# Kernel tuning notes

Hardware: AMD Instinct MI355X
Metric: run time of the kernel (lower is better)

## Reference

```python
import jax, jax.numpy as jnp
import numpy as np

BQ = 64  # query block size
BK = 64  # key block size
PV_SCALE = 1e-3  # pvthreshd (~0..50) -> prob threshold, mirrors int8 P-quantization cutoff


def setup_inputs() -> dict:
    key = jax.random.key(0)
    ks = jax.random.split(key, 6)
    B, H, L, D = 2, 16, 2048, 64
    q = jax.random.normal(ks[0], (B, H, L, D), jnp.float32)
    k = jax.random.normal(ks[1], (B, H, L, D), jnp.float32)
    v = jax.random.normal(ks[2], (B, H, L, D), jnp.float32)
    # per-head tuned thresholds (init defaults / autotune ranges)
    cdfthreshd = 0.85 + 0.14 * jax.random.uniform(ks[3], (H,), jnp.float32)
    simthreshd1 = jax.random.uniform(ks[4], (H,), jnp.float32, minval=-0.3, maxval=0.5)
    pvthreshd = jax.random.uniform(ks[5], (H,), jnp.float32, minval=15.0, maxval=25.0)
    return dict(q=q, k=k, v=v, cdfthreshd=cdfthreshd,
                simthreshd1=simthreshd1, pvthreshd=pvthreshd)


def _sparse_meansim_attention(q, k, v, cdfthreshd, simthreshd1, pvthreshd):
    B, H, L, D = q.shape
    nqb, nkb = L // BQ, L // BK
    scale = 1.0 / jnp.sqrt(jnp.float32(D))

    # smooth_k: subtract per-(B,H) key mean along sequence
    k = k - k.mean(axis=2, keepdims=True)

    qb = q.reshape(B, H, nqb, BQ, D)
    kb = k.reshape(B, H, nkb, BK, D)
    qm = qb.mean(axis=3)  # [B,H,nqb,D]
    km = kb.mean(axis=3)  # [B,H,nkb,D]

    # mean cosine similarity of queries to their block mean -> pooled (prunable) blocks
    qn = jnp.linalg.norm(qb, axis=-1)            # [B,H,nqb,BQ]
    qmn = jnp.linalg.norm(qm, axis=-1)           # [B,H,nqb]
    cos = jnp.einsum('bhnqd,bhnd->bhnq', qb, qm) / (qn * qmn[..., None] + 1e-6)
    pooled = cos.mean(axis=-1) > simthreshd1[None, :, None]  # [B,H,nqb]

    # block-level score map from pooled means, CDF-based top-mass block selection
    s = jnp.einsum('bhid,bhjd->bhij', qm, km) * scale        # [B,H,nqb,nkb]
    p = jax.nn.softmax(s, axis=-1)
    order = jnp.argsort(-p, axis=-1)
    p_sorted = jnp.take_along_axis(p, order, axis=-1)
    excl_cdf = jnp.cumsum(p_sorted, axis=-1) - p_sorted      # exclusive CDF
    keep_sorted = excl_cdf < cdfthreshd[None, :, None, None]
    keep = jnp.take_along_axis(keep_sorted, jnp.argsort(order, axis=-1), axis=-1)

    sink = (jnp.arange(nkb) == 0)  # attention_sink: always keep first key block
    block_mask = keep | (~pooled)[..., None] | sink          # [B,H,nqb,nkb]

    # full attention restricted to selected blocks
    S = jnp.einsum('bhqd,bhkd->bhqk', q, k) * scale          # [B,H,L,L]
    m = jnp.repeat(jnp.repeat(block_mask, BQ, axis=2), BK, axis=3)
    P = jax.nn.softmax(jnp.where(m, S, -jnp.inf), axis=-1)

    # second-stage PV pruning: skip PV accumulation for negligible prob blocks
    Pb = P.reshape(B, H, nqb, BQ, nkb, BK)
    pv_keep = Pb.max(axis=(3, 5)) >= pvthreshd[None, :, None, None] * PV_SCALE
    pv_keep = pv_keep | sink
    Pb = Pb * pv_keep[:, :, :, None, :, None].astype(P.dtype)

    o = jnp.einsum('bhqk,bhkd->bhqd', Pb.reshape(B, H, L, L), v)
    return o


def reference(q, k, v, cdfthreshd, simthreshd1, pvthreshd):
    return _sparse_meansim_attention(q, k, v, cdfthreshd, simthreshd1, pvthreshd)
```

## Files before the change

### kernel.cpp

```cpp
#include <hip/hip_runtime.h>
#include <hip/hip_bf16.h>
#include <math.h>
#include <stdint.h>

#define B 2
#define H 16
#define L 2048
#define D 64
#define NB 32

typedef unsigned short u16;
typedef unsigned int u32;
typedef __attribute__((ext_vector_type(2))) unsigned int u32x2;
typedef __attribute__((ext_vector_type(4))) unsigned int u32x4;
typedef __attribute__((ext_vector_type(8))) short s16x8;
typedef __attribute__((ext_vector_type(4))) float f32x4;

union FragU { s16x8 v; u32 u[4]; };

#if defined(__has_builtin)
#if __has_builtin(__builtin_amdgcn_exp2f)
#define EXP2F __builtin_amdgcn_exp2f
#else
#define EXP2F exp2f
#endif
#else
#define EXP2F exp2f
#endif
#define LOG2E 1.4426950408889634f
#define C1SC 0.18033688011112042f

__device__ __forceinline__ u32 pkbf(float a, float b) {
  __hip_bfloat162 h = __float22bfloat162_rn(make_float2(a, b));
  union { __hip_bfloat162 h; u32 u; } cv; cv.h = h; return cv.u;
}
__device__ __forceinline__ float bf2f(u32 u16bits) {
  union { u32 u; float f; } c; c.u = u16bits << 16; return c.f;
}
__device__ __forceinline__ void split4(float4 p, u32x2& hi, u32x2& lo) {
  u32 h01 = pkbf(p.x, p.y), h23 = pkbf(p.z, p.w);
  float rx = p.x - bf2f(h01 & 0xffffu);
  float ry = p.y - bf2f(h01 >> 16);
  float rz = p.z - bf2f(h23 & 0xffffu);
  float rw = p.w - bf2f(h23 >> 16);
  hi = (u32x2){h01, h23};
  lo = (u32x2){pkbf(rx, ry), pkbf(rz, rw)};
}
__device__ __forceinline__ int swz(int row, int colb) {
  return (row << 7) + (colb ^ ((row & 7) << 4));
}

__global__ __launch_bounds__(256) void k_prep(const float* __restrict__ k,
                                              const float* __restrict__ v,
                                              float* __restrict__ ksum,
                                              u16* __restrict__ khi_g,
                                              u16* __restrict__ klo_g,
                                              u16* __restrict__ vthi_g,
                                              u16* __restrict__ vtlo_g,
                                              float* __restrict__ kbmax) {
  int blk0 = blockIdx.x, t = threadIdx.x;
  int xcd = blk0 & 7, sidx = blk0 >> 3;
  int bh = xcd * 4 + (sidx >> 5), j = sidx & 31;
  int blk = bh * 32 + j;
  int lane = t & 63, w = t >> 6;
  __shared__ float vt[64 * 65];
  __shared__ float pk_[4][64];
  __shared__ unsigned bmaxS;
  if (t == 0) bmaxS = 0u;
  size_t base = (size_t)blk * 4096;

  int r0 = t >> 3;
  int c8 = (t & 7) * 8;
  float cs[8] = {0.f, 0.f, 0.f, 0.f, 0.f, 0.f, 0.f, 0.f};
  float rmax = 0.f;
#pragma unroll
  for (int it = 0; it < 2; ++it) {
    int r = r0 + 32 * it;
    const float* kp = k + base + r * 64 + c8;
    float4 f0 = *(const float4*)kp;
    float4 f1 = *(const float4*)(kp + 4);
    u32x2 h0, l0, h1, l1;
    split4(f0, h0, l0); split4(f1, h1, l1);
    *(u32x4*)(khi_g + base + r * 64 + c8) = (u32x4){h0[0], h0[1], h1[0], h1[1]};
    *(u32x4*)(klo_g + base + r * 64 + c8) = (u32x4){l0[0], l0[1], l1[0], l1[1]};
    cs[0] += f0.x; cs[1] += f0.y; cs[2] += f0.z; cs[3] += f0.w;
    cs[4] += f1.x; cs[5] += f1.y; cs[6] += f1.z; cs[7] += f1.w;
    float ssq = f0.x*f0.x + f0.y*f0.y + f0.z*f0.z + f0.w*f0.w
              + f1.x*f1.x + f1.y*f1.y + f1.z*f1.z + f1.w*f1.w;
    ssq += __shfl_xor(ssq, 1); ssq += __shfl_xor(ssq, 2); ssq += __shfl_xor(ssq, 4);
    if ((t & 7) == 0) rmax = fmaxf(rmax, ssq);
    const float* vp = v + base + r * 64 + c8;
    float4 g0 = *(const float4*)vp;
    float4 g1 = *(const float4*)(vp + 4);
    vt[(c8 + 0) * 65 + r] = g0.x;
    vt[(c8 + 1) * 65 + r] = g0.y;
    vt[(c8 + 2) * 65 + r] = g0.z;
    vt[(c8 + 3) * 65 + r] = g0.w;
    vt[(c8 + 4) * 65 + r] = g1.x;
    vt[(c8 + 5) * 65 + r] = g1.y;
    vt[(c8 + 6) * 65 + r] = g1.z;
    vt[(c8 + 7) * 65 + r] = g1.w;
  }
  if ((t & 7) == 0) atomicMax(&bmaxS, __float_as_uint(rmax));
#pragma unroll
  for (int i = 0; i < 8; ++i) {
    cs[i] += __shfl_xor(cs[i], 8);
    cs[i] += __shfl_xor(cs[i], 16);
    cs[i] += __shfl_xor(cs[i], 32);
  }
  if (lane < 8) {
    *(float4*)&pk_[w][lane * 8]     = (float4){cs[0], cs[1], cs[2], cs[3]};
    *(float4*)&pk_[w][lane * 8 + 4] = (float4){cs[4], cs[5], cs[6], cs[7]};
  }
  __syncthreads();
  if (t < 64) ksum[(size_t)blk * 64 + t] = pk_[0][t] + pk_[1][t] + pk_[2][t] + pk_[3][t];
  if (t == 0) kbmax[blk] = __uint_as_float(bmaxS);
#pragma unroll
  for (int it = 0; it < 2; ++it) {
    int idx = t + 256 * it, d = idx >> 3, s8 = (idx & 7) * 8;
    const float* vr = &vt[d * 65 + s8];
    float4 f0 = {vr[0], vr[1], vr[2], vr[3]};
    float4 f1 = {vr[4], vr[5], vr[6], vr[7]};
    u32x2 h0, l0, h1, l1;
    split4(f0, h0, l0); split4(f1, h1, l1);
    size_t o = (size_t)bh * 131072 + (size_t)d * 2048 + j * 64 + s8;
    *(u32x4*)(vthi_g + o) = (u32x4){h0[0], h0[1], h1[0], h1[1]};
    *(u32x4*)(vtlo_g + o) = (u32x4){l0[0], l0[1], l1[0], l1[1]};
  }
}

__global__ __launch_bounds__(256, 2) void k_attn(
    const float* __restrict__ q,
    const float* __restrict__ ksum,
    const u16* __restrict__ khi_g, const u16* __restrict__ klo_g,
    const u16* __restrict__ vthi_g, const u16* __restrict__ vtlo_g,
    const float* __restrict__ cdfthreshd, const float* __restrict__ simthreshd1,
    const float* __restrict__ pvthreshd, const float* __restrict__ kbmax,
    float* __restrict__ out) {
  int blk0 = blockIdx.x;
  int blk = (blk0 & 7) * 64 + (blk0 >> 3);
  int bh = blk >> 4, ip = blk & 15, h = bh & (H - 1);
  int t = threadIdx.x, lane = t & 63, w = t >> 6;
  int m16 = lane & 15, quad = lane >> 4;

  __shared__ __align__(16) uint8_t smem[65568];
  u32*   rbm0  = (u32*)smem;
  float* lpart = (float*)(smem + 16896);
  float* qmS   = (float*)(smem + 18944);
  float* MSs   = (float*)(smem + 19456);
  float* linvS = (float*)(smem + 19968);
  int*   flg   = (int*)(smem + 65536);
#define PHB(qb, b) (smem + (qb) * 32768 + (b) * 16384)
#define PLB(qb, b) (smem + (qb) * 32768 + (b) * 16384 + 8192)

  const float* qg0 = q + ((size_t)bh * L + (size_t)(2 * ip) * 64) * D;
  const float* qg1 = qg0 + 64 * D;
  const u16* kh = khi_g + (size_t)bh * (L * D);
  const u16* kl = klo_g + (size_t)bh * (L * D);
  const u16* vh = vthi_g + (size_t)bh * (L * D);
  const u16* vl = vtlo_g + (size_t)bh * (L * D);

  s16x8 qhf[2][4][2], qlf[2][4][2];
#pragma unroll
  for (int qb = 0; qb < 2; ++qb) {
    const float* qgq = qb ? qg1 : qg0;
#pragma unroll
    for (int nt = 0; nt < 4; ++nt)
#pragma unroll
      for (int ks = 0; ks < 2; ++ks) {
        const float* p0 = qgq + (16 * nt + m16) * 64 + ks * 32 + quad * 8;
        float4 a = *(const float4*)p0;
        float4 b2 = *(const float4*)(p0 + 4);
        u32x2 ha, la, hb, lb;
        split4(a, ha, la); split4(b2, hb, lb);
        FragU fh, fl;
        fh.u[0] = ha[0]; fh.u[1] = ha[1]; fh.u[2] = hb[0]; fh.u[3] = hb[1];
        fl.u[0] = la[0]; fl.u[1] = la[1]; fl.u[2] = lb[0]; fl.u[3] = lb[1];
        qhf[qb][nt][ks] = fh.v; qlf[qb][nt][ks] = fl.v;
      }
  }
  for (int e = t; e < 2 * 64 * 33; e += 256)
    rbm0[e] = 0x7F800000u;

  if (w == 0 || w == 2) {
    int qb = w >> 1;
    const float* qgq = qb ? qg1 : qg0;
    float s = 0.f;
    for (int r = 0; r < 64; ++r) s += qgq[r * 64 + lane];
    qmS[qb * 64 + lane] = s * (1.f / 64.f);
  }
  if (w == 1) {
    float m = (lane < 32) ? kbmax[bh * 32 + lane] : 0.f;
    for (int off = 16; off; off >>= 1) m = fmaxf(m, __shfl_xor(m, off, 32));
    if (lane == 0) ((float*)flg)[6] = m;
  }
  __syncthreads();

  bool keepj = false;
  if ((w == 0 || w == 2) && lane < 32) {
    int qb = w >> 1, j = lane;
    const float* qmv = qmS + qb * 64;
    const float* ksp = ksum + (size_t)bh * NB * 64 + j * 64;
    float sv = 0.f;
    for (int d = 0; d < 64; ++d) sv += qmv[d] * ksp[d];
    sv *= (1.f / 64.f) * 0.125f;
    float mx = sv;
    for (int off = 16; off; off >>= 1) mx = fmaxf(mx, __shfl_xor(mx, off, 32));
    float p = expf(sv - mx);
    float sum = p;
    for (int off = 16; off; off >>= 1) sum += __shfl_xor(sum, off, 32);
    p /= sum;
    float excl = 0.f;
    for (int u = 0; u < 32; ++u) {
      float pu = __shfl(p, u, 32);
      if ((pu > p) || (pu == p && u < j)) excl += pu;
    }
    keepj = excl < cdfthreshd[h];
  }
  if (w == 1 || w == 3) {
    int qb = w >> 1, r = lane;
    const float* qgq = qb ? qg1 : qg0;
    const float* qmv = qmS + qb * 64;
    float kmax2 = ((float*)flg)[6];
    float dot = 0.f, qn2 = 0.f, qmn2 = 0.f;
    for (int d = 0; d < 64; ++d) {
      float a = qgq[r * 64 + d], b2 = qmv[d];
      dot += a * b2; qn2 += a * a; qmn2 += b2 * b2;
    }
    float cs = dot / (sqrtf(qn2) * sqrtf(qmn2) + 1e-6f);
    float su = cs;
    for (int off = 32; off; off >>= 1) su += __shfl_xor(su, off);
    if (lane == 0) flg[qb] = (su * (1.f / 64.f)) > simthreshd1[h];
    MSs[qb * 64 + r] = sqrtf(qn2 * kmax2) * 0.125f;
  }
  __syncthreads();
  if ((w == 0 || w == 2) && lane < 32) {
    int qb = w >> 1;
    bool bit = keepj || !flg[qb] || (lane == 0);
    unsigned long long bal = __ballot(bit);
    if (lane == 0) flg[2 + qb] = (int)(u32)bal;
  }
  __syncthreads();
  u32 mw0 = (u32)flg[2], mw1 = (u32)flg[3];

  float Mq[2][4];
#pragma unroll
  for (int qb = 0; qb < 2; ++qb)
#pragma unroll
    for (int nt = 0; nt < 4; ++nt) Mq[qb][nt] = MSs[qb * 64 + 16 * nt + m16] * LOG2E;

  float lp[2][4] = {{0.f,0.f,0.f,0.f},{0.f,0.f,0.f,0.f}};
  {
    u32 mwU = mw0 | mw1;
    int j = (int)__builtin_ctz(mwU);
    u32 rm_ = mwU & (mwU - 1);
    s16x8 ka[2][2], kan[2][2];
    {
      const u16* kr0 = kh + (size_t)(j * 64 + 16 * w + m16) * 64 + quad * 8;
      const u16* kl0 = kl + (size_t)(j * 64 + 16 * w + m16) * 64 + quad * 8;
#pragma unroll
      for (int ks = 0; ks < 2; ++ks) {
        ka[ks][0] = *(const s16x8*)(kr0 + ks * 32);
        ka[ks][1] = *(const s16x8*)(kl0 + ks * 32);
      }
    }
    for (;;) {
      int nj = -1;
      if (rm_) {
        nj = (int)__builtin_ctz(rm_); rm_ &= rm_ - 1;
        const u16* nr = kh + (size_t)(nj * 64 + 16 * w + m16) * 64 + quad * 8;
        const u16* nl = kl + (size_t)(nj * 64 + 16 * w + m16) * 64 + quad * 8;
#pragma unroll
        for (int ks = 0; ks < 2; ++ks) {
          kan[ks][0] = *(const s16x8*)(nr + ks * 32);
          kan[ks][1] = *(const s16x8*)(nl + ks * 32);
        }
      }
#pragma unroll
      for (int qb = 0; qb < 2; ++qb) {
        u32 mm = qb ? mw1 : mw0;
        if (!((mm >> j) & 1u)) continue;
        f32x4 acc[4];
#pragma unroll
        for (int nt = 0; nt < 4; ++nt) acc[nt] = (f32x4){0.f, 0.f, 0.f, 0.f};
        __builtin_amdgcn_s_setprio(1);
#pragma unroll
        for (int ks = 0; ks < 2; ++ks)
#pragma unroll
          for (int nt = 0; nt < 4; ++nt) {
            acc[nt] = __builtin_amdgcn_mfma_f32_16x16x32_bf16(ka[ks][0], qhf[qb][nt][ks], acc[nt], 0, 0, 0);
            acc[nt] = __builtin_amdgcn_mfma_f32_16x16x32_bf16(ka[ks][1], qhf[qb][nt][ks], acc[nt], 0, 0, 0);
            acc[nt] = __builtin_amdgcn_mfma_f32_16x16x32_bf16(ka[ks][0], qlf[qb][nt][ks], acc[nt], 0, 0, 0);
          }
        __builtin_amdgcn_s_setprio(0);
#pragma unroll
        for (int nt = 0; nt < 4; ++nt) {
          float vmax = -1e30f;
#pragma unroll
          for (int reg = 0; reg < 4; ++reg) {
            float s = fmaf(acc[nt][reg], C1SC, -Mq[qb][nt]);
            lp[qb][nt] += EXP2F(s);
            vmax = fmaxf(vmax, s);
          }
          vmax = fmaxf(vmax, __shfl_xor(vmax, 16));
          vmax = fmaxf(vmax, __shfl_xor(vmax, 32));
          if (quad == 0)
            atomicMin(rbm0 + qb * (64 * 33) + (16 * nt + m16) * 33 + j,
                      __float_as_uint(fmaxf(-vmax, 0.f)));
        }
      }
      if (nj < 0) break;
#pragma unroll
      for (int ks = 0; ks < 2; ++ks) { ka[ks][0] = kan[ks][0]; ka[ks][1] = kan[ks][1]; }
      j = nj;
    }
  }
#pragma unroll
  for (int qb = 0; qb < 2; ++qb)
#pragma unroll
    for (int nt = 0; nt < 4; ++nt) {
      float s = lp[qb][nt];
      s += __shfl_xor(s, 16); s += __shfl_xor(s, 32);
      if (quad == 0) lpart[w * 128 + qb * 64 + 16 * nt + m16] = s;
    }
  __syncthreads();
  if (t < 128) linvS[t] = 1.f / (lpart[t] + lpart[128 + t] + lpart[256 + t] + lpart[384 + t]);
  __syncthreads();

  if (w < 2 && lane < 32) {
    u32 mm = w ? mw1 : mw0;
    bool keep = (mm >> lane) & 1u;
    if (keep && lane != 0) {
      float thr = pvthreshd[h] * 1e-3f;
      const float* lin = linvS + w * 64;
      const u32* rb = rbm0 + w * (64 * 33);
      float mp = 0.f;
      for (int r = 0; r < 64; ++r) {
        float key = __uint_as_float(rb[r * 33 + lane]);
        mp = fmaxf(mp, EXP2F(-key) * lin[r]);
      }
      keep = mp >= thr;
    }
    unsigned long long bal = __ballot(keep);
    if (lane == 0) flg[4 + w] = (int)(u32)bal;
  }
  __syncthreads();
  u32 gm0 = (u32)flg[4], gm1 = (u32)flg[5];

  float linq[2][4];
#pragma unroll
  for (int qb = 0; qb < 2; ++qb)
#pragma unroll
    for (int nt = 0; nt < 4; ++nt) linq[qb][nt] = linvS[qb * 64 + 16 * nt + m16];
  f32x4 oacc[2][4];
#pragma unroll
  for (int qb = 0; qb < 2; ++qb)
#pragma unroll
    for (int nt = 0; nt < 4; ++nt) oacc[qb][nt] = (f32x4){0.f, 0.f, 0.f, 0.f};
  __syncthreads();

  {
    u32 gmU = gm0 | gm1;
    int j = -1;
    u32 g2 = gmU;
    int buf = 0;
    s16x8 ka[2][2];
    if (g2) {
      j = (int)__builtin_ctz(g2); g2 &= g2 - 1;
      const u16* kr0 = kh + (size_t)(j * 64 + 16 * w + m16) * 64 + quad * 8;
      const u16* kl0 = kl + (size_t)(j * 64 + 16 * w + m16) * 64 + quad * 8;
#pragma unroll
      for (int ks = 0; ks < 2; ++ks) {
        ka[ks][0] = *(const s16x8*)(kr0 + ks * 32);
        ka[ks][1] = *(const s16x8*)(kl0 + ks * 32);
      }
    }
    while (j >= 0) {
      int in0 = (gm0 >> j) & 1, in1 = (gm1 >> j) & 1;
      s16x8 va[2][2];
      {
        const u16* vr0 = vh + (size_t)(16 * w + m16) * L + j * 64 + quad * 8;
        const u16* vl0 = vl + (size_t)(16 * w + m16) * L + j * 64 + quad * 8;
#pragma unroll
        for (int ks = 0; ks < 2; ++ks) {
          va[ks][0] = *(const s16x8*)(vr0 + ks * 32);
          va[ks][1] = *(const s16x8*)(vl0 + ks * 32);
        }
      }
      f32x4 acc[4];
#pragma unroll
      for (int qb = 0; qb < 2; ++qb) {
        if (!(qb ? in1 : in0)) continue;
#pragma unroll
        for (int nt = 0; nt < 4; ++nt) acc[nt] = (f32x4){0.f, 0.f, 0.f, 0.f};
        __builtin_amdgcn_s_setprio(1);
#pragma unroll
        for (int ks = 0; ks < 2; ++ks)
#pragma unroll
          for (int nt = 0; nt < 4; ++nt) {
            acc[nt] = __builtin_amdgcn_mfma_f32_16x16x32_bf16(ka[ks][0], qhf[qb][nt][ks], acc[nt], 0, 0, 0);
            acc[nt] = __builtin_amdgcn_mfma_f32_16x16x32_bf16(ka[ks][1], qhf[qb][nt][ks], acc[nt], 0, 0, 0);
            acc[nt] = __builtin_amdgcn_mfma_f32_16x16x32_bf16(ka[ks][0], qlf[qb][nt][ks], acc[nt], 0, 0, 0);
          }
        __builtin_amdgcn_s_setprio(0);
#pragma unroll
        for (int nt = 0; nt < 4; ++nt) {
          float4 pv;
          pv.x = EXP2F(fmaf(acc[nt][0], C1SC, -Mq[qb][nt])) * linq[qb][nt];
          pv.y = EXP2F(fmaf(acc[nt][1], C1SC, -Mq[qb][nt])) * linq[qb][nt];
          pv.z = EXP2F(fmaf(acc[nt][2], C1SC, -Mq[qb][nt])) * linq[qb][nt];
          pv.w = EXP2F(fmaf(acc[nt][3], C1SC, -Mq[qb][nt])) * linq[qb][nt];
          u32x2 hi, lo; split4(pv, hi, lo);
          int off = swz(16 * nt + m16, 32 * w + 8 * quad);
          *(u32x2*)(PHB(qb, buf) + off) = hi;
          *(u32x2*)(PLB(qb, buf) + off) = lo;
        }
      }
      int nj = -1;
      if (g2) {
        nj = (int)__builtin_ctz(g2); g2 &= g2 - 1;
        const u16* nr = kh + (size_t)(nj * 64 + 16 * w + m16) * 64 + quad * 8;
        const u16* nl = kl + (size_t)(nj * 64 + 16 * w + m16) * 64 + quad * 8;
#pragma unroll
        for (int ks = 0; ks < 2; ++ks) {
          ka[ks][0] = *(const s16x8*)(nr + ks * 32);
          ka[ks][1] = *(const s16x8*)(nl + ks * 32);
        }
      }
      __syncthreads();
#pragma unroll
      for (int qb = 0; qb < 2; ++qb) {
        if (!(qb ? in1 : in0)) continue;
        const uint8_t* ph_ = PHB(qb, buf);
        const uint8_t* pl_ = PLB(qb, buf);
#pragma unroll
        for (int ks = 0; ks < 2; ++ks)
#pragma unroll
          for (int nt = 0; nt < 4; ++nt) {
            s16x8 pbh = *(const s16x8*)(ph_ + swz(16 * nt + m16, ks * 64 + quad * 16));
            s16x8 pbl = *(const s16x8*)(pl_ + swz(16 * nt + m16, ks * 64 + quad * 16));
            __builtin_amdgcn_s_setprio(1);
            oacc[qb][nt] = __builtin_amdgcn_mfma_f32_16x16x32_bf16(va[ks][0], pbh, oacc[qb][nt], 0, 0, 0);
            oacc[qb][nt] = __builtin_amdgcn_mfma_f32_16x16x32_bf16(va[ks][1], pbh, oacc[qb][nt], 0, 0, 0);
            oacc[qb][nt] = __builtin_amdgcn_mfma_f32_16x16x32_bf16(va[ks][0], pbl, oacc[qb][nt], 0, 0, 0);
            __builtin_amdgcn_s_setprio(0);
          }
      }
      buf ^= 1;
      j = nj;
    }
  }

#pragma unroll
  for (int qb = 0; qb < 2; ++qb) {
    float* ob = out + ((size_t)bh * L + (size_t)(2 * ip + qb) * 64) * D;
#pragma unroll
    for (int nt = 0; nt < 4; ++nt)
      __builtin_nontemporal_store(oacc[qb][nt],
          (f32x4*)(ob + (16 * nt + m16) * 64 + 16 * w + 4 * quad));
  }
}

extern "C" void kernel_launch(void* const* d_in, const int* in_sizes, int n_in,
                              void* d_out, int out_size, void* d_ws, size_t ws_size,
                              hipStream_t stream) {
  (void)in_sizes; (void)n_in; (void)out_size; (void)ws_size;
  const float* q   = (const float*)d_in[0];
  const float* k   = (const float*)d_in[1];
  const float* v   = (const float*)d_in[2];
  const float* cdf = (const float*)d_in[3];
  const float* sim = (const float*)d_in[4];
  const float* pvt = (const float*)d_in[5];
  float* out = (float*)d_out;

  uint8_t* w8 = (uint8_t*)d_ws;
  float* ksum  = (float*)w8;
  float* kbmax = (float*)(w8 + 262144);
  u16* khi_g  = (u16*)(w8 + 266240);
  u16* klo_g  = khi_g + (size_t)B * H * L * D;
  u16* vthi_g = klo_g + (size_t)B * H * L * D;
  u16* vtlo_g = vthi_g + (size_t)B * H * L * D;

  k_prep<<<B * H * NB, 256, 0, stream>>>(k, v, ksum, khi_g, klo_g, vthi_g, vtlo_g, kbmax);
  k_attn<<<B * H * NB / 2, 256, 0, stream>>>(q, ksum, khi_g, klo_g, vthi_g, vtlo_g,
                                             cdf, sim, pvt, kbmax, out);
}
```

Before: 197.9 us.

## Fuse PV into first pass, then subtract pruned blocks in a correction pass

The attention kernel now accumulates unnormalized P·V for every mask-selected block during the first QK pass, instead of running a separate second QK+PV pass over the surviving blocks. After the row sums and PV-pruning decisions are known, a correction pass recomputes QK only for blocks pruned by the pv threshold and subtracts their contribution. The output is scaled by the inverse row sum at store time. This avoids recomputing QK for kept blocks, at the cost of doing PV work for blocks later pruned, extra LDS (a swizzled row-max buffer), and possible cancellation error from the subtraction.

```diff
diff --git a/kernel.cpp b/kernel.cpp
--- a/kernel.cpp
+++ b/kernel.cpp
@@ -48,6 +48,9 @@
 }
 __device__ __forceinline__ int swz(int row, int colb) {
   return (row << 7) + (colb ^ ((row & 7) << 4));
+}
+__device__ __forceinline__ int rbmix(int qb, int row, int j) {
+  return qb * 2048 + row * 32 + (j ^ (row & 31));
 }
 
 __global__ __launch_bounds__(256) void k_prep(const float* __restrict__ k,
@@ -143,13 +146,14 @@
   int t = threadIdx.x, lane = t & 63, w = t >> 6;
   int m16 = lane & 15, quad = lane >> 4;
 
-  __shared__ __align__(16) uint8_t smem[65568];
-  u32*   rbm0  = (u32*)smem;
-  float* lpart = (float*)(smem + 16896);
-  float* qmS   = (float*)(smem + 18944);
-  float* MSs   = (float*)(smem + 19456);
-  float* linvS = (float*)(smem + 19968);
-  int*   flg   = (int*)(smem + 65536);
+  __shared__ __align__(16) uint8_t smem[81920];
+  u32*   rbm    = (u32*)(smem + 65536);
+  float* qmS    = (float*)smem;
+  float* MSs    = (float*)(smem + 512);
+  int*   preFlg = (int*)(smem + 1024);
+  float* lpart  = (float*)(smem + 16384);
+  float* linvS  = (float*)(smem + 18432);
+  int*   postFlg= (int*)(smem + 18944);
 #define PHB(qb, b) (smem + (qb) * 32768 + (b) * 16384)
 #define PLB(qb, b) (smem + (qb) * 32768 + (b) * 16384 + 8192)
 
@@ -179,8 +183,7 @@
         qhf[qb][nt][ks] = fh.v; qlf[qb][nt][ks] = fl.v;
       }
   }
-  for (int e = t; e < 2 * 64 * 33; e += 256)
-    rbm0[e] = 0x7F800000u;
+  for (int e = t; e < 2 * 64 * 32; e += 256) rbm[e] = 0x7F800000u;
 
   if (w == 0 || w == 2) {
     int qb = w >> 1;
@@ -192,7 +195,7 @@
   if (w == 1) {
     float m = (lane < 32) ? kbmax[bh * 32 + lane] : 0.f;
     for (int off = 16; off; off >>= 1) m = fmaxf(m, __shfl_xor(m, off, 32));
-    if (lane == 0) ((float*)flg)[6] = m;
+    if (lane == 0) ((float*)preFlg)[6] = m;
   }
   __syncthreads();
 
@@ -221,7 +224,7 @@
     int qb = w >> 1, r = lane;
     const float* qgq = qb ? qg1 : qg0;
     const float* qmv = qmS + qb * 64;
-    float kmax2 = ((float*)flg)[6];
+    float kmax2 = ((float*)preFlg)[6];
     float dot = 0.f, qn2 = 0.f, qmn2 = 0.f;
     for (int d = 0; d < 64; ++d) {
       float a = qgq[r * 64 + d], b2 = qmv[d];
@@ -230,31 +233,38 @@
     float cs = dot / (sqrtf(qn2) * sqrtf(qmn2) + 1e-6f);
     float su = cs;
     for (int off = 32; off; off >>= 1) su += __shfl_xor(su, off);
-    if (lane == 0) flg[qb] = (su * (1.f / 64.f)) > simthreshd1[h];
+    if (lane == 0) preFlg[qb] = (su * (1.f / 64.f)) > simthreshd1[h];
     MSs[qb * 64 + r] = sqrtf(qn2 * kmax2) * 0.125f;
   }
   __syncthreads();
   if ((w == 0 || w == 2) && lane < 32) {
     int qb = w >> 1;
-    bool bit = keepj || !flg[qb] || (lane == 0);
+    bool bit = keepj || !preFlg[qb] || (lane == 0);
     unsigned long long bal = __ballot(bit);
-    if (lane == 0) flg[2 + qb] = (int)(u32)bal;
-  }
-  __syncthreads();
-  u32 mw0 = (u32)flg[2], mw1 = (u32)flg[3];
+    if (lane == 0) preFlg[2 + qb] = (int)(u32)bal;
+  }
+  __syncthreads();
+  u32 mw0 = (u32)preFlg[2], mw1 = (u32)preFlg[3];
 
   float Mq[2][4];
 #pragma unroll
   for (int qb = 0; qb < 2; ++qb)
 #pragma unroll
     for (int nt = 0; nt < 4; ++nt) Mq[qb][nt] = MSs[qb * 64 + 16 * nt + m16] * LOG2E;
-
   float lp[2][4] = {{0.f,0.f,0.f,0.f},{0.f,0.f,0.f,0.f}};
+  f32x4 oacc[2][4];
+#pragma unroll
+  for (int qb = 0; qb < 2; ++qb)
+#pragma unroll
+    for (int nt = 0; nt < 4; ++nt) oacc[qb][nt] = (f32x4){0.f, 0.f, 0.f, 0.f};
+  __syncthreads();
+
   {
     u32 mwU = mw0 | mw1;
     int j = (int)__builtin_ctz(mwU);
     u32 rm_ = mwU & (mwU - 1);
-    s16x8 ka[2][2], kan[2][2];
+    int buf = 0;
+    s16x8 ka[2][2];
     {
       const u16* kr0 = kh + (size_t)(j * 64 + 16 * w + m16) * 64 + quad * 8;
       const u16* kl0 = kl + (size_t)(j * 64 + 16 * w + m16) * 64 + quad * 8;
@@ -265,160 +275,91 @@
       }
     }
     for (;;) {
+      int in0 = (mw0 >> j) & 1, in1 = (mw1 >> j) & 1;
+      s16x8 va[2][2];
+      f32x4 acc[4];
+      if (in0) {
+#pragma unroll
+        for (int nt = 0; nt < 4; ++nt) acc[nt] = (f32x4){0.f, 0.f, 0.f, 0.f};
+        __builtin_amdgcn_s_setprio(1);
+#pragma unroll
+        for (int ks = 0; ks < 2; ++ks)
+#pragma unroll
+          for (int nt = 0; nt < 4; ++nt) {
+            acc[nt] = __builtin_amdgcn_mfma_f32_16x16x32_bf16(ka[ks][0], qhf[0][nt][ks], acc[nt], 0, 0, 0);
+            acc[nt] = __builtin_amdgcn_mfma_f32_16x16x32_bf16(ka[ks][1], qhf[0][nt][ks], acc[nt], 0, 0, 0);
+            acc[nt] = __builtin_amdgcn_mfma_f32_16x16x32_bf16(ka[ks][0], qlf[0][nt][ks], acc[nt], 0, 0, 0);
+          }
+        __builtin_amdgcn_s_setprio(0);
+#pragma unroll
+        for (int nt = 0; nt < 4; ++nt) {
+          float vmax = -1e30f;
+          float4 pv;
+#pragma unroll
+          for (int reg = 0; reg < 4; ++reg) {
+            float s = fmaf(acc[nt][reg], C1SC, -Mq[0][nt]);
+            float e = EXP2F(s);
+            lp[0][nt] += e;
+            vmax = fmaxf(vmax, s);
+            ((float*)&pv)[reg] = e;
+          }
+          vmax = fmaxf(vmax, __shfl_xor(vmax, 16));
+          vmax = fmaxf(vmax, __shfl_xor(vmax, 32));
+          if (quad == 0)
+            atomicMin(rbm + rbmix(0, 16 * nt + m16, j), __float_as_uint(fmaxf(-vmax, 0.f)));
+          u32x2 hi, lo; split4(pv, hi, lo);
+          int off = swz(16 * nt + m16, 32 * w + 8 * quad);
+          *(u32x2*)(PHB(0, buf) + off) = hi;
+          *(u32x2*)(PLB(0, buf) + off) = lo;
+        }
+      }
+      {
+        const u16* vr0 = vh + (size_t)(16 * w + m16) * L + j * 64 + quad * 8;
+        const u16* vl0 = vl + (size_t)(16 * w + m16) * L + j * 64 + quad * 8;
+#pragma unroll
+        for (int ks = 0; ks < 2; ++ks) {
+          va[ks][0] = *(const s16x8*)(vr0 + ks * 32);
+          va[ks][1] = *(const s16x8*)(vl0 + ks * 32);
+        }
+      }
+      if (in1) {
+#pragma unroll
+        for (int nt = 0; nt < 4; ++nt) acc[nt] = (f32x4){0.f, 0.f, 0.f, 0.f};
+        __builtin_amdgcn_s_setprio(1);
+#pragma unroll
+        for (int ks = 0; ks < 2; ++ks)
+#pragma unroll
+          for (int nt = 0; nt < 4; ++nt) {
+            acc[nt] = __builtin_amdgcn_mfma_f32_16x16x32_bf16(ka[ks][0], qhf[1][nt][ks], acc[nt], 0, 0, 0);
+            acc[nt] = __builtin_amdgcn_mfma_f32_16x16x32_bf16(ka[ks][1], qhf[1][nt][ks], acc[nt], 0, 0, 0);
+            acc[nt] = __builtin_amdgcn_mfma_f32_16x16x32_bf16(ka[ks][0], qlf[1][nt][ks], acc[nt], 0, 0, 0);
+          }
+        __builtin_amdgcn_s_setprio(0);
+#pragma unroll
+        for (int nt = 0; nt < 4; ++nt) {
+          float vmax = -1e30f;
+          float4 pv;
+#pragma unroll
+          for (int reg = 0; reg < 4; ++reg) {
+            float s = fmaf(acc[nt][reg], C1SC, -Mq[1][nt]);
+            float e = EXP2F(s);
+            lp[1][nt] += e;
+            vmax = fmaxf(vmax, s);
+            ((float*)&pv)[reg] = e;
+          }
+          vmax = fmaxf(vmax, __shfl_xor(vmax, 16));
+          vmax = fmaxf(vmax, __shfl_xor(vmax, 32));
+          if (quad == 0)
+            atomicMin(rbm + rbmix(1, 16 * nt + m16, j), __float_as_uint(fmaxf(-vmax, 0.f)));
+          u32x2 hi, lo; split4(pv, hi, lo);
+          int off = swz(16 * nt + m16, 32 * w + 8 * quad);
+          *(u32x2*)(PHB(1, buf) + off) = hi;
+          *(u32x2*)(PLB(1, buf) + off) = lo;
+        }
+      }
       int nj = -1;
       if (rm_) {
         nj = (int)__builtin_ctz(rm_); rm_ &= rm_ - 1;
-        const u16* nr = kh + (size_t)(nj * 64 + 16 * w + m16) * 64 + quad * 8;
-        const u16* nl = kl + (size_t)(nj * 64 + 16 * w + m16) * 64 + quad * 8;
-#pragma unroll
-        for (int ks = 0; ks < 2; ++ks) {
-          kan[ks][0] = *(const s16x8*)(nr + ks * 32);
-          kan[ks][1] = *(const s16x8*)(nl + ks * 32);
-        }
-      }
-#pragma unroll
-      for (int qb = 0; qb < 2; ++qb) {
-        u32 mm = qb ? mw1 : mw0;
-        if (!((mm >> j) & 1u)) continue;
-        f32x4 acc[4];
-#pragma unroll
-        for (int nt = 0; nt < 4; ++nt) acc[nt] = (f32x4){0.f, 0.f, 0.f, 0.f};
-        __builtin_amdgcn_s_setprio(1);
-#pragma unroll
-        for (int ks = 0; ks < 2; ++ks)
-#pragma unroll
-          for (int nt = 0; nt < 4; ++nt) {
-            acc[nt] = __builtin_amdgcn_mfma_f32_16x16x32_bf16(ka[ks][0], qhf[qb][nt][ks], acc[nt], 0, 0, 0);
-            acc[nt] = __builtin_amdgcn_mfma_f32_16x16x32_bf16(ka[ks][1], qhf[qb][nt][ks], acc[nt], 0, 0, 0);
-            acc[nt] = __builtin_amdgcn_mfma_f32_16x16x32_bf16(ka[ks][0], qlf[qb][nt][ks], acc[nt], 0, 0, 0);
-          }
-        __builtin_amdgcn_s_setprio(0);
-#pragma unroll
-        for (int nt = 0; nt < 4; ++nt) {
-          float vmax = -1e30f;
-#pragma unroll
-          for (int reg = 0; reg < 4; ++reg) {
-            float s = fmaf(acc[nt][reg], C1SC, -Mq[qb][nt]);
-            lp[qb][nt] += EXP2F(s);
-            vmax = fmaxf(vmax, s);
-          }
-          vmax = fmaxf(vmax, __shfl_xor(vmax, 16));
-          vmax = fmaxf(vmax, __shfl_xor(vmax, 32));
-          if (quad == 0)
-            atomicMin(rbm0 + qb * (64 * 33) + (16 * nt + m16) * 33 + j,
-                      __float_as_uint(fmaxf(-vmax, 0.f)));
-        }
-      }
-      if (nj < 0) break;
-#pragma unroll
-      for (int ks = 0; ks < 2; ++ks) { ka[ks][0] = kan[ks][0]; ka[ks][1] = kan[ks][1]; }
-      j = nj;
-    }
-  }
-#pragma unroll
-  for (int qb = 0; qb < 2; ++qb)
-#pragma unroll
-    for (int nt = 0; nt < 4; ++nt) {
-      float s = lp[qb][nt];
-      s += __shfl_xor(s, 16); s += __shfl_xor(s, 32);
-      if (quad == 0) lpart[w * 128 + qb * 64 + 16 * nt + m16] = s;
-    }
-  __syncthreads();
-  if (t < 128) linvS[t] = 1.f / (lpart[t] + lpart[128 + t] + lpart[256 + t] + lpart[384 + t]);
-  __syncthreads();
-
-  if (w < 2 && lane < 32) {
-    u32 mm = w ? mw1 : mw0;
-    bool keep = (mm >> lane) & 1u;
-    if (keep && lane != 0) {
-      float thr = pvthreshd[h] * 1e-3f;
-      const float* lin = linvS + w * 64;
-      const u32* rb = rbm0 + w * (64 * 33);
-      float mp = 0.f;
-      for (int r = 0; r < 64; ++r) {
-        float key = __uint_as_float(rb[r * 33 + lane]);
-        mp = fmaxf(mp, EXP2F(-key) * lin[r]);
-      }
-      keep = mp >= thr;
-    }
-    unsigned long long bal = __ballot(keep);
-    if (lane == 0) flg[4 + w] = (int)(u32)bal;
-  }
-  __syncthreads();
-  u32 gm0 = (u32)flg[4], gm1 = (u32)flg[5];
-
-  float linq[2][4];
-#pragma unroll
-  for (int qb = 0; qb < 2; ++qb)
-#pragma unroll
-    for (int nt = 0; nt < 4; ++nt) linq[qb][nt] = linvS[qb * 64 + 16 * nt + m16];
-  f32x4 oacc[2][4];
-#pragma unroll
-  for (int qb = 0; qb < 2; ++qb)
-#pragma unroll
-    for (int nt = 0; nt < 4; ++nt) oacc[qb][nt] = (f32x4){0.f, 0.f, 0.f, 0.f};
-  __syncthreads();
-
-  {
-    u32 gmU = gm0 | gm1;
-    int j = -1;
-    u32 g2 = gmU;
-    int buf = 0;
-    s16x8 ka[2][2];
-    if (g2) {
-      j = (int)__builtin_ctz(g2); g2 &= g2 - 1;
-      const u16* kr0 = kh + (size_t)(j * 64 + 16 * w + m16) * 64 + quad * 8;
-      const u16* kl0 = kl + (size_t)(j * 64 + 16 * w + m16) * 64 + quad * 8;
-#pragma unroll
-      for (int ks = 0; ks < 2; ++ks) {
-        ka[ks][0] = *(const s16x8*)(kr0 + ks * 32);
-        ka[ks][1] = *(const s16x8*)(kl0 + ks * 32);
-      }
-    }
-    while (j >= 0) {
-      int in0 = (gm0 >> j) & 1, in1 = (gm1 >> j) & 1;
-      s16x8 va[2][2];
-      {
-        const u16* vr0 = vh + (size_t)(16 * w + m16) * L + j * 64 + quad * 8;
-        const u16* vl0 = vl + (size_t)(16 * w + m16) * L + j * 64 + quad * 8;
-#pragma unroll
-        for (int ks = 0; ks < 2; ++ks) {
-          va[ks][0] = *(const s16x8*)(vr0 + ks * 32);
-          va[ks][1] = *(const s16x8*)(vl0 + ks * 32);
-        }
-      }
-      f32x4 acc[4];
-#pragma unroll
-      for (int qb = 0; qb < 2; ++qb) {
-        if (!(qb ? in1 : in0)) continue;
-#pragma unroll
-        for (int nt = 0; nt < 4; ++nt) acc[nt] = (f32x4){0.f, 0.f, 0.f, 0.f};
-        __builtin_amdgcn_s_setprio(1);
-#pragma unroll
-        for (int ks = 0; ks < 2; ++ks)
-#pragma unroll
-          for (int nt = 0; nt < 4; ++nt) {
-            acc[nt] = __builtin_amdgcn_mfma_f32_16x16x32_bf16(ka[ks][0], qhf[qb][nt][ks], acc[nt], 0, 0, 0);
-            acc[nt] = __builtin_amdgcn_mfma_f32_16x16x32_bf16(ka[ks][1], qhf[qb][nt][ks], acc[nt], 0, 0, 0);
-            acc[nt] = __builtin_amdgcn_mfma_f32_16x16x32_bf16(ka[ks][0], qlf[qb][nt][ks], acc[nt], 0, 0, 0);
-          }
-        __builtin_amdgcn_s_setprio(0);
-#pragma unroll
-        for (int nt = 0; nt < 4; ++nt) {
-          float4 pv;
-          pv.x = EXP2F(fmaf(acc[nt][0], C1SC, -Mq[qb][nt])) * linq[qb][nt];
-          pv.y = EXP2F(fmaf(acc[nt][1], C1SC, -Mq[qb][nt])) * linq[qb][nt];
-          pv.z = EXP2F(fmaf(acc[nt][2], C1SC, -Mq[qb][nt])) * linq[qb][nt];
-          pv.w = EXP2F(fmaf(acc[nt][3], C1SC, -Mq[qb][nt])) * linq[qb][nt];
-          u32x2 hi, lo; split4(pv, hi, lo);
-          int off = swz(16 * nt + m16, 32 * w + 8 * quad);
-          *(u32x2*)(PHB(qb, buf) + off) = hi;
-          *(u32x2*)(PLB(qb, buf) + off) = lo;
-        }
-      }
-      int nj = -1;
-      if (g2) {
-        nj = (int)__builtin_ctz(g2); g2 &= g2 - 1;
         const u16* nr = kh + (size_t)(nj * 64 + 16 * w + m16) * 64 + quad * 8;
         const u16* nl = kl + (size_t)(nj * 64 + 16 * w + m16) * 64 + quad * 8;
 #pragma unroll
@@ -446,18 +387,148 @@
             __builtin_amdgcn_s_setprio(0);
           }
       }
+      if (nj < 0) break;
       buf ^= 1;
       j = nj;
     }
   }
+  __syncthreads();
+
+#pragma unroll
+  for (int qb = 0; qb < 2; ++qb)
+#pragma unroll
+    for (int nt = 0; nt < 4; ++nt) {
+      float s = lp[qb][nt];
+      s += __shfl_xor(s, 16); s += __shfl_xor(s, 32);
+      if (quad == 0) lpart[w * 128 + qb * 64 + 16 * nt + m16] = s;
+    }
+  __syncthreads();
+  if (t < 128) linvS[t] = 1.f / (lpart[t] + lpart[128 + t] + lpart[256 + t] + lpart[384 + t]);
+  __syncthreads();
+
+  if (w < 2 && lane < 32) {
+    u32 mm = w ? mw1 : mw0;
+    bool keep = (mm >> lane) & 1u;
+    if (keep && lane != 0) {
+      float thr = pvthreshd[h] * 1e-3f;
+      const float* lin = linvS + w * 64;
+      float mp = 0.f;
+      for (int r = 0; r < 64; ++r) {
+        float key = __uint_as_float(rbm[rbmix(w, r, lane)]);
+        mp = fmaxf(mp, EXP2F(-key) * lin[r]);
+      }
+      keep = mp >= thr;
+    }
+    unsigned long long bal = __ballot(keep);
+    if (lane == 0) postFlg[w] = (int)(u32)bal;
+  }
+  __syncthreads();
+  u32 gm0 = (u32)postFlg[0], gm1 = (u32)postFlg[1];
+  u32 cm0 = mw0 & ~gm0, cm1 = mw1 & ~gm1;
+
+  {
+    u32 cmU = cm0 | cm1;
+    int j = -1;
+    u32 g2 = cmU;
+    s16x8 ka[2][2];
+    if (g2) {
+      j = (int)__builtin_ctz(g2); g2 &= g2 - 1;
+      const u16* kr0 = kh + (size_t)(j * 64 + 16 * w + m16) * 64 + quad * 8;
+      const u16* kl0 = kl + (size_t)(j * 64 + 16 * w + m16) * 64 + quad * 8;
+#pragma unroll
+      for (int ks = 0; ks < 2; ++ks) {
+        ka[ks][0] = *(const s16x8*)(kr0 + ks * 32);
+        ka[ks][1] = *(const s16x8*)(kl0 + ks * 32);
+      }
+    }
+    while (j >= 0) {
+      int in0 = (cm0 >> j) & 1, in1 = (cm1 >> j) & 1;
+      s16x8 va[2][2];
+      {
+        const u16* vr0 = vh + (size_t)(16 * w + m16) * L + j * 64 + quad * 8;
+        const u16* vl0 = vl + (size_t)(16 * w + m16) * L + j * 64 + quad * 8;
+#pragma unroll
+        for (int ks = 0; ks < 2; ++ks) {
+          va[ks][0] = *(const s16x8*)(vr0 + ks * 32);
+          va[ks][1] = *(const s16x8*)(vl0 + ks * 32);
+        }
+      }
+      __syncthreads();
+#pragma unroll
+      for (int qb = 0; qb < 2; ++qb) {
+        if (!(qb ? in1 : in0)) continue;
+        f32x4 acc[4];
+#pragma unroll
+        for (int nt = 0; nt < 4; ++nt) acc[nt] = (f32x4){0.f, 0.f, 0.f, 0.f};
+        __builtin_amdgcn_s_setprio(1);
+#pragma unroll
+        for (int ks = 0; ks < 2; ++ks)
+#pragma unroll
+          for (int nt = 0; nt < 4; ++nt) {
+            acc[nt] = __builtin_amdgcn_mfma_f32_16x16x32_bf16(ka[ks][0], qhf[qb][nt][ks], acc[nt], 0, 0, 0);
+            acc[nt] = __builtin_amdgcn_mfma_f32_16x16x32_bf16(ka[ks][1], qhf[qb][nt][ks], acc[nt], 0, 0, 0);
+            acc[nt] = __builtin_amdgcn_mfma_f32_16x16x32_bf16(ka[ks][0], qlf[qb][nt][ks], acc[nt], 0, 0, 0);
+          }
+        __builtin_amdgcn_s_setprio(0);
+#pragma unroll
+        for (int nt = 0; nt < 4; ++nt) {
+          float4 pv;
+#pragma unroll
+          for (int reg = 0; reg < 4; ++reg) {
+            float s = fmaf(acc[nt][reg], C1SC, -Mq[qb][nt]);
+            ((float*)&pv)[reg] = -EXP2F(s);
+          }
+          u32x2 hi, lo; split4(pv, hi, lo);
+          int off = swz(16 * nt + m16, 32 * w + 8 * quad);
+          *(u32x2*)(PHB(qb, 0) + off) = hi;
+          *(u32x2*)(PLB(qb, 0) + off) = lo;
+        }
+      }
+      int nj = -1;
+      if (g2) {
+        nj = (int)__builtin_ctz(g2); g2 &= g2 - 1;
+        const u16* nr = kh + (size_t)(nj * 64 + 16 * w + m16) * 64 + quad * 8;
+        const u16* nl = kl + (size_t)(nj * 64 + 16 * w + m16) * 64 + quad * 8;
+#pragma unroll
+        for (int ks = 0; ks < 2; ++ks) {
+          ka[ks][0] = *(const s16x8*)(nr + ks * 32);
+          ka[ks][1] = *(const s16x8*)(nl + ks * 32);
+        }
+      }
+      __syncthreads();
+#pragma unroll
+      for (int qb = 0; qb < 2; ++qb) {
+        if (!(qb ? in1 : in0)) continue;
+        const uint8_t* ph_ = PHB(qb, 0);
+        const uint8_t* pl_ = PLB(qb, 0);
+#pragma unroll
+        for (int ks = 0; ks < 2; ++ks)
+#pragma unroll
+          for (int nt = 0; nt < 4; ++nt) {
+            s16x8 pbh = *(const s16x8*)(ph_ + swz(16 * nt + m16, ks * 64 + quad * 16));
+            s16x8 pbl = *(const s16x8*)(pl_ + swz(16 * nt + m16, ks * 64 + quad * 16));
+            __builtin_amdgcn_s_setprio(1);
+            oacc[qb][nt] = __builtin_amdgcn_mfma_f32_16x16x32_bf16(va[ks][0], pbh, oacc[qb][nt], 0, 0, 0);
+            oacc[qb][nt] = __builtin_amdgcn_mfma_f32_16x16x32_bf16(va[ks][1], pbh, oacc[qb][nt], 0, 0, 0);
+            oacc[qb][nt] = __builtin_amdgcn_mfma_f32_16x16x32_bf16(va[ks][0], pbl, oacc[qb][nt], 0, 0, 0);
+            __builtin_amdgcn_s_setprio(0);
+          }
+      }
+      j = nj;
+    }
+  }
 
 #pragma unroll
   for (int qb = 0; qb < 2; ++qb) {
     float* ob = out + ((size_t)bh * L + (size_t)(2 * ip + qb) * 64) * D;
 #pragma unroll
-    for (int nt = 0; nt < 4; ++nt)
-      __builtin_nontemporal_store(oacc[qb][nt],
+    for (int nt = 0; nt < 4; ++nt) {
+      float lin = linvS[qb * 64 + 16 * nt + m16];
+      f32x4 o = oacc[qb][nt];
+      o[0] *= lin; o[1] *= lin; o[2] *= lin; o[3] *= lin;
+      __builtin_nontemporal_store(o,
           (f32x4*)(ob + (16 * nt + m16) * 64 + 16 * w + 4 * quad));
+    }
   }
 }
 
```

Result: slower. 310.5 us (+56.9%).
